# Kernel optimization log

Hardware: AMD Instinct MI355X
Metric: run time of the kernel (lower is better)

The kernel has to match this reference:

```python
import jax, jax.numpy as jnp
import numpy as np

INPUT_DIM = 1024
HIDDEN = 1024
MASKED = INPUT_DIM // 2  # even indices are the conditioning half
BATCH = 65536


def setup_inputs() -> dict:
    key = jax.random.key(0)
    ks = jax.random.split(key, 7)
    s1 = 1.0 / np.sqrt(MASKED)
    s2 = 1.0 / np.sqrt(HIDDEN)
    x = jax.random.normal(ks[0], (BATCH, INPUT_DIM), dtype=jnp.float32)
    W1 = jax.random.uniform(ks[1], (MASKED, HIDDEN), jnp.float32, -s1, s1)
    b1 = jax.random.uniform(ks[2], (HIDDEN,), jnp.float32, -s1, s1)
    W2 = jax.random.uniform(ks[3], (HIDDEN, HIDDEN), jnp.float32, -s2, s2)
    b2 = jax.random.uniform(ks[4], (HIDDEN,), jnp.float32, -s2, s2)
    W3 = jax.random.uniform(ks[5], (HIDDEN, INPUT_DIM - MASKED), jnp.float32, -s2, s2)
    b3 = jax.random.uniform(ks[6], (INPUT_DIM - MASKED,), jnp.float32, -s2, s2)
    return {"x": x, "W1": W1, "b1": b1, "W2": W2, "b2": b2, "W3": W3, "b3": b3}


def reference(x, W1, b1, W2, b2, W3, b3):
    # mask_type='even': mask[::2]=1 -> even indices conditioning, odd indices translated
    masked = x[:, 0::2]  # [B, MASKED], gather of conditioning half
    h = jax.nn.relu(masked @ W1 + b1)
    h = jax.nn.relu(h @ W2 + b2)
    translation = h @ W3 + b3  # [B, INPUT_DIM - MASKED]
    # scatter-add translation into odd positions
    y = x.at[:, 1::2].add(translation)
    return y
```

## Files before the change

### kernel.cpp

```cpp
#include <hip/hip_runtime.h>
#include <stdint.h>

#define BATCH  65536
#define IN_DIM 1024
#define MASKED 512
#define HIDDEN 1024

typedef unsigned short u16;
typedef __bf16 bf16x8 __attribute__((ext_vector_type(8)));
typedef float  f32x4  __attribute__((ext_vector_type(4)));

typedef __attribute__((address_space(1))) void gvoid;
typedef __attribute__((address_space(3))) void lvoid;

__device__ __forceinline__ u16 f32_to_bf16(float f) {
    union { float f; uint32_t u; } v; v.f = f;
    uint32_t r = v.u + 0x7FFFu + ((v.u >> 16) & 1u);
    return (u16)(r >> 16);
}

__global__ void prep_xm(const float* __restrict__ x, u16* __restrict__ xm) {
    int idx = blockIdx.x * blockDim.x + threadIdx.x;
    const float4* xv = reinterpret_cast<const float4*>(x);
    float4 v0 = xv[idx * 2];
    float4 v1 = xv[idx * 2 + 1];
    ushort4 o;
    o.x = f32_to_bf16(v0.x);
    o.y = f32_to_bf16(v0.z);
    o.z = f32_to_bf16(v1.x);
    o.w = f32_to_bf16(v1.z);
    reinterpret_cast<ushort4*>(xm)[idx] = o;
}

__global__ void wconv(const float* __restrict__ W, u16* __restrict__ Wt,
                      int K, int N) {
    __shared__ float t[32][33];
    const int nbk = K / 32;
    const int bk = blockIdx.x % nbk;
    const int bn = blockIdx.x / nbk;
    const int tx = threadIdx.x & 31;
    const int ty = threadIdx.x >> 5;
    const int k0 = bk * 32, n0 = bn * 32;
    #pragma unroll
    for (int i = 0; i < 4; ++i)
        t[ty + i * 8][tx] = W[(int64_t)(k0 + ty + i * 8) * N + n0 + tx];
    __syncthreads();
    #pragma unroll
    for (int i = 0; i < 4; ++i)
        Wt[(int64_t)(n0 + ty + i * 8) * K + k0 + tx] = f32_to_bf16(t[tx][ty + i * 8]);
}

template<int K, int N, int MODE>
__global__ __launch_bounds__(256, 4)
void gemm_bt(const u16* __restrict__ A, const u16* __restrict__ Bt,
             const float* __restrict__ bias,
             u16* __restrict__ Cb,
             const float* __restrict__ X,
             float* __restrict__ Y) {
    constexpr int BK = 64;
    __shared__ u16 As[128 * BK];
    __shared__ u16 Bs[128 * BK];

    const int tid  = threadIdx.x;
    const int lane = tid & 63;
    const int w    = tid >> 6;
    const int wr   = w >> 1;
    const int wc   = w & 1;

    const int nwg = gridDim.x;
    const int cpx = nwg >> 3;
    const int bid = (blockIdx.x & 7) * cpx + (blockIdx.x >> 3);

    constexpr int nbn = N / 128;
    const int bm = bid / nbn;
    const int bn = bid % nbn;
    const int m0 = bm * 128;
    const int n0 = bn * 128;

    f32x4 acc[4][4];
    #pragma unroll
    for (int i = 0; i < 4; ++i)
        #pragma unroll
        for (int j = 0; j < 4; ++j)
            acc[i][j] = f32x4{0.f, 0.f, 0.f, 0.f};

    const int srow = lane >> 3;
    const int scol = ((lane & 7) ^ srow) * 8;
    const u16* aptr = A  + (int64_t)(m0 + w * 32 + srow) * K + scol;
    const u16* bptr = Bt + (int64_t)(n0 + w * 32 + srow) * K + scol;

    const int rxor = lane & 7;
    const int q0   = lane >> 4;

    for (int kt = 0; kt < K / BK; ++kt) {
        __syncthreads();
        const int koff = kt * BK;
        #pragma unroll
        for (int c = 0; c < 4; ++c) {
            __builtin_amdgcn_global_load_lds(
                (gvoid*)(aptr + koff + c * 8 * K),
                (lvoid*)(&As[(w * 32 + c * 8) * BK]), 16, 0, 0);
            __builtin_amdgcn_global_load_lds(
                (gvoid*)(bptr + koff + c * 8 * K),
                (lvoid*)(&Bs[(w * 32 + c * 8) * BK]), 16, 0, 0);
        }
        __syncthreads();

        #pragma unroll
        for (int kk = 0; kk < 2; ++kk) {
            const int kcol = ((kk * 4 + q0) ^ rxor) * 8;
            bf16x8 a[4], b[4];
            #pragma unroll
            for (int i = 0; i < 4; ++i)
                a[i] = *reinterpret_cast<const bf16x8*>(
                    &As[(wr * 64 + i * 16 + (lane & 15)) * BK + kcol]);
            #pragma unroll
            for (int j = 0; j < 4; ++j)
                b[j] = *reinterpret_cast<const bf16x8*>(
                    &Bs[(wc * 64 + j * 16 + (lane & 15)) * BK + kcol]);
            #pragma unroll
            for (int i = 0; i < 4; ++i)
                #pragma unroll
                for (int j = 0; j < 4; ++j)
                    acc[i][j] = __builtin_amdgcn_mfma_f32_16x16x32_bf16(
                        a[i], b[j], acc[i][j], 0, 0, 0);
        }
    }

    const int cl = lane & 15;
    const int rg = (lane >> 4) * 4;
    #pragma unroll
    for (int j = 0; j < 4; ++j) {
        const int n  = n0 + wc * 64 + j * 16 + cl;
        const float bv = bias[n];
        #pragma unroll
        for (int i = 0; i < 4; ++i) {
            #pragma unroll
            for (int r = 0; r < 4; ++r) {
                const int m = m0 + wr * 64 + i * 16 + rg + r;
                float v = acc[i][j][r] + bv;
                if (MODE == 0) {
                    v = v > 0.f ? v : 0.f;
                    Cb[(int64_t)m * N + n] = f32_to_bf16(v);
                } else {
                    const int64_t p = (int64_t)m * IN_DIM + 2 * n;
                    float2 xv = *reinterpret_cast<const float2*>(&X[p]);
                    float2 o;
                    o.x = xv.x;
                    o.y = xv.y + v;
                    *reinterpret_cast<float2*>(&Y[p]) = o;
                }
            }
        }
    }
}

extern "C" void kernel_launch(void* const* d_in, const int* in_sizes, int n_in,
                              void* d_out, int out_size, void* d_ws, size_t ws_size,
                              hipStream_t stream) {
    const float* x  = (const float*)d_in[0];
    const float* W1 = (const float*)d_in[1];
    const float* b1 = (const float*)d_in[2];
    const float* W2 = (const float*)d_in[3];
    const float* b2 = (const float*)d_in[4];
    const float* W3 = (const float*)d_in[5];
    const float* b3 = (const float*)d_in[6];
    float* y = (float*)d_out;

    char* ws = (char*)d_ws;
    u16* h1  = (u16*)(ws);
    u16* h2  = (u16*)(ws + 134217728);
    u16* xm  = (u16*)(ws + 134217728);
    u16* W1t = (u16*)(ws + 268435456);
    u16* W2t = (u16*)(ws + 268435456 + 1048576);
    u16* W3t = (u16*)(ws + 268435456 + 1048576 + 2097152);

    prep_xm<<<BATCH * IN_DIM / 8 / 256, 256, 0, stream>>>(x, xm);

    wconv<<<(MASKED / 32) * (HIDDEN / 32), 256, 0, stream>>>(W1, W1t, MASKED, HIDDEN);
    wconv<<<(HIDDEN / 32) * (HIDDEN / 32), 256, 0, stream>>>(W2, W2t, HIDDEN, HIDDEN);
    wconv<<<(HIDDEN / 32) * ((IN_DIM - MASKED) / 32), 256, 0, stream>>>(W3, W3t, HIDDEN, IN_DIM - MASKED);

    gemm_bt<MASKED, HIDDEN, 0><<<(BATCH / 128) * (HIDDEN / 128), 256, 0, stream>>>(
        xm, W1t, b1, h1, nullptr, nullptr);
    gemm_bt<HIDDEN, HIDDEN, 0><<<(BATCH / 128) * (HIDDEN / 128), 256, 0, stream>>>(
        h1, W2t, b2, h2, nullptr, nullptr);
    gemm_bt<HIDDEN, IN_DIM - MASKED, 1><<<(BATCH / 128) * ((IN_DIM - MASKED) / 128), 256, 0, stream>>>(
        h2, W3t, b3, nullptr, x, y);
}
```

Measured before the change: 443.1 us.

## Fuse even-column gather and bf16 conversion into first GEMM; merge weight conversions

Removes the separate prep_xm pass and has the first GEMM read fp32 x directly, pick the even columns and pack them to bf16 in registers before storing to LDS. The three weight-conversion launches are also merged into a single launch. This saves one full read of x plus the write and re-read of the bf16 staging buffer, and two launch overheads. In exchange, GEMM1 now loads twice the bytes of A per tile (full fp32 rows, half of which are discarded) through registers instead of direct-to-LDS loads, which may lengthen its load phase.

```diff
diff --git a/kernel.cpp b/kernel.cpp
--- a/kernel.cpp
+++ b/kernel.cpp
@@ -19,25 +19,25 @@
     return (u16)(r >> 16);
 }
 
-__global__ void prep_xm(const float* __restrict__ x, u16* __restrict__ xm) {
-    int idx = blockIdx.x * blockDim.x + threadIdx.x;
-    const float4* xv = reinterpret_cast<const float4*>(x);
-    float4 v0 = xv[idx * 2];
-    float4 v1 = xv[idx * 2 + 1];
-    ushort4 o;
-    o.x = f32_to_bf16(v0.x);
-    o.y = f32_to_bf16(v0.z);
-    o.z = f32_to_bf16(v1.x);
-    o.w = f32_to_bf16(v1.z);
-    reinterpret_cast<ushort4*>(xm)[idx] = o;
-}
-
-__global__ void wconv(const float* __restrict__ W, u16* __restrict__ Wt,
-                      int K, int N) {
+__device__ __forceinline__ uint32_t cvtpk_bf16(float a, float b) {
+    uint32_t r;
+    asm("v_cvt_pk_bf16_f32 %0, %1, %2" : "=v"(r) : "v"(a), "v"(b));
+    return r;
+}
+
+__global__ void wconv_all(const float* __restrict__ W1, const float* __restrict__ W2,
+                          const float* __restrict__ W3,
+                          u16* __restrict__ W1t, u16* __restrict__ W2t,
+                          u16* __restrict__ W3t) {
     __shared__ float t[32][33];
+    int bid = blockIdx.x;
+    const float* W; u16* Wt; int K, N;
+    if (bid < 512)       { W = W1; Wt = W1t; K = 512;  N = 1024; }
+    else if (bid < 1536) { W = W2; Wt = W2t; K = 1024; N = 1024; bid -= 512; }
+    else                 { W = W3; Wt = W3t; K = 1024; N = 512;  bid -= 1536; }
     const int nbk = K / 32;
-    const int bk = blockIdx.x % nbk;
-    const int bn = blockIdx.x / nbk;
+    const int bk = bid % nbk;
+    const int bn = bid / nbk;
     const int tx = threadIdx.x & 31;
     const int ty = threadIdx.x >> 5;
     const int k0 = bk * 32, n0 = bn * 32;
@@ -48,6 +48,112 @@
     #pragma unroll
     for (int i = 0; i < 4; ++i)
         Wt[(int64_t)(n0 + ty + i * 8) * K + k0 + tx] = f32_to_bf16(t[tx][ty + i * 8]);
+}
+
+__global__ __launch_bounds__(256, 4)
+void gemm_g1(const float* __restrict__ X,
+             const u16* __restrict__ Bt,
+             const float* __restrict__ bias,
+             u16* __restrict__ Cb) {
+    constexpr int K = MASKED;
+    constexpr int N = HIDDEN;
+    constexpr int BK = 64;
+    __shared__ u16 As[128 * BK];
+    __shared__ u16 Bs[128 * BK];
+
+    const int tid  = threadIdx.x;
+    const int lane = tid & 63;
+    const int w    = tid >> 6;
+    const int wr   = w >> 1;
+    const int wc   = w & 1;
+
+    const int nwg = gridDim.x;
+    const int cpx = nwg >> 3;
+    const int bid = (blockIdx.x & 7) * cpx + (blockIdx.x >> 3);
+    constexpr int nbn = N / 128;
+    const int bm = bid / nbn;
+    const int bn = bid % nbn;
+    const int m0 = bm * 128;
+    const int n0 = bn * 128;
+
+    f32x4 acc[4][4];
+    #pragma unroll
+    for (int i = 0; i < 4; ++i)
+        #pragma unroll
+        for (int j = 0; j < 4; ++j)
+            acc[i][j] = f32x4{0.f, 0.f, 0.f, 0.f};
+
+    const int srow = lane >> 3;
+    const int jch  = lane & 7;
+    const int gch  = jch ^ srow;
+    const u16* bptr = Bt + (int64_t)(n0 + w * 32 + srow) * K + gch * 8;
+    const float* xptr = X + (int64_t)(m0 + w * 32 + srow) * IN_DIM + gch * 16;
+    const int ldsA = (w * 32 + srow) * BK + jch * 8;
+
+    const int rxor = lane & 7;
+    const int q0   = lane >> 4;
+
+    for (int kt = 0; kt < K / BK; ++kt) {
+        __syncthreads();
+        #pragma unroll
+        for (int c = 0; c < 4; ++c)
+            __builtin_amdgcn_global_load_lds(
+                (gvoid*)(bptr + kt * BK + c * 8 * K),
+                (lvoid*)(&Bs[(w * 32 + c * 8) * BK]), 16, 0, 0);
+        #pragma unroll
+        for (int c = 0; c < 4; ++c) {
+            const float* xp = xptr + (int64_t)c * 8 * IN_DIM + kt * 128;
+            float4 f0 = *reinterpret_cast<const float4*>(xp);
+            float4 f1 = *reinterpret_cast<const float4*>(xp + 4);
+            float4 f2 = *reinterpret_cast<const float4*>(xp + 8);
+            float4 f3 = *reinterpret_cast<const float4*>(xp + 12);
+            uint4 r;
+            r.x = cvtpk_bf16(f0.x, f0.z);
+            r.y = cvtpk_bf16(f1.x, f1.z);
+            r.z = cvtpk_bf16(f2.x, f2.z);
+            r.w = cvtpk_bf16(f3.x, f3.z);
+            *reinterpret_cast<uint4*>(&As[ldsA + c * 8 * BK]) = r;
+        }
+        __syncthreads();
+
+        #pragma unroll
+        for (int kk = 0; kk < 2; ++kk) {
+            const int kcol = ((kk * 4 + q0) ^ rxor) * 8;
+            bf16x8 a[4], b[4];
+            #pragma unroll
+            for (int i = 0; i < 4; ++i)
+                a[i] = *reinterpret_cast<const bf16x8*>(
+                    &As[(wr * 64 + i * 16 + (lane & 15)) * BK + kcol]);
+            #pragma unroll
+            for (int j = 0; j < 4; ++j)
+                b[j] = *reinterpret_cast<const bf16x8*>(
+                    &Bs[(wc * 64 + j * 16 + (lane & 15)) * BK + kcol]);
+            #pragma unroll
+            for (int i = 0; i < 4; ++i)
+                #pragma unroll
+                for (int j = 0; j < 4; ++j)
+                    acc[i][j] = __builtin_amdgcn_mfma_f32_16x16x32_bf16(
+                        a[i], b[j], acc[i][j], 0, 0, 0);
+        }
+    }
+
+    const int cl = lane & 15;
+    const int rg = (lane >> 4) * 4;
+    #pragma unroll
+    for (int j = 0; j < 4; ++j) {
+        const int n  = n0 + wc * 64 + j * 16 + cl;
+        const float bv = bias[n];
+        #pragma unroll
+        for (int i = 0; i < 4; ++i) {
+            #pragma unroll
+            for (int r = 0; r < 4; ++r) {
+                const int m = m0 + wr * 64 + i * 16 + rg + r;
+                float v = acc[i][j][r] + bv;
+                v = v > 0.f ? v : 0.f;
+                Cb[(int64_t)m * N + n] = f32_to_bf16(v);
+            }
+        }
+    }
 }
 
 template<int K, int N, int MODE>
@@ -170,19 +276,14 @@
     char* ws = (char*)d_ws;
     u16* h1  = (u16*)(ws);
     u16* h2  = (u16*)(ws + 134217728);
-    u16* xm  = (u16*)(ws + 134217728);
     u16* W1t = (u16*)(ws + 268435456);
     u16* W2t = (u16*)(ws + 268435456 + 1048576);
     u16* W3t = (u16*)(ws + 268435456 + 1048576 + 2097152);
 
-    prep_xm<<<BATCH * IN_DIM / 8 / 256, 256, 0, stream>>>(x, xm);
-
-    wconv<<<(MASKED / 32) * (HIDDEN / 32), 256, 0, stream>>>(W1, W1t, MASKED, HIDDEN);
-    wconv<<<(HIDDEN / 32) * (HIDDEN / 32), 256, 0, stream>>>(W2, W2t, HIDDEN, HIDDEN);
-    wconv<<<(HIDDEN / 32) * ((IN_DIM - MASKED) / 32), 256, 0, stream>>>(W3, W3t, HIDDEN, IN_DIM - MASKED);
-
-    gemm_bt<MASKED, HIDDEN, 0><<<(BATCH / 128) * (HIDDEN / 128), 256, 0, stream>>>(
-        xm, W1t, b1, h1, nullptr, nullptr);
+    wconv_all<<<2048, 256, 0, stream>>>(W1, W2, W3, W1t, W2t, W3t);
+
+    gemm_g1<<<(BATCH / 128) * (HIDDEN / 128), 256, 0, stream>>>(x, W1t, b1, h1);
+
     gemm_bt<HIDDEN, HIDDEN, 0><<<(BATCH / 128) * (HIDDEN / 128), 256, 0, stream>>>(
         h1, W2t, b2, h2, nullptr, nullptr);
     gemm_bt<HIDDEN, IN_DIM - MASKED, 1><<<(BATCH / 128) * ((IN_DIM - MASKED) / 128), 256, 0, stream>>>(
```

Measured after the change: 600.5 us. 35.5% more time.
